# Kernel optimization log

Measured on AMD Instinct MI355X. Metric: run time of the kernel, lower is better.

The kernel has to match this reference:

```python
import jax, jax.numpy as jnp
import numpy as np

V = 256        # vocab (bytes)
DM = 1024      # d_model
NL = 8         # num layers
N = 16         # d_state
K = 4          # d_conv
E = 2 * DM     # d_inner (expand=2)
R = DM // 16   # dt_rank = 64
EPS = 1e-5
B, T = 1, 1024


def setup_inputs() -> dict:
    key = jax.random.key(0)
    ks = jax.random.split(key, 10)
    s = lambda i, shape, scale=0.02: jax.random.normal(ks[i], shape, jnp.float32) * scale
    A_init = jnp.log(jnp.tile(jnp.arange(1, N + 1, dtype=jnp.float32), (NL, E, 1)))
    return {
        "input_ids": jax.random.randint(ks[0], (B, T), 0, V),
        "embed": s(1, (V, DM)),
        "Wxz": s(2, (NL, DM, 2 * E)),            # in_proj (no bias)
        "conv_w": s(3, (NL, E, K), 0.1),          # depthwise causal conv
        "conv_b": jnp.zeros((NL, E), jnp.float32),
        "Wx": s(4, (NL, E, R + 2 * N)),           # x_proj -> dt, B, C
        "Wdt": s(5, (NL, R, E), 0.1),             # dt_proj
        "dt_bias": jnp.full((NL, E), -4.6, jnp.float32),  # softplus(-4.6) ~ 0.01
        "A_log": A_init,                          # A = -exp(A_log), S4D-real init
        "D": jnp.ones((NL, E), jnp.float32),      # skip connection
        "Wout": s(6, (NL, E, DM)),                # out_proj (no bias)
        "norm_w": jnp.ones((NL, DM), jnp.float32),
        "final_norm_w": jnp.ones((DM,), jnp.float32),
        "lm_head_w": s(7, (DM, V)),               # lm_head (no bias)
    }


def rmsnorm(x, w):
    return x * jax.lax.rsqrt(jnp.mean(x * x, axis=-1, keepdims=True) + EPS) * w


def selective_scan(x, dt, A, Bm, Cm, Dp):
    # x, dt: [B,T,E]; A: [E,N]; Bm, Cm: [B,T,N]; Dp: [E]
    dA = jnp.exp(dt[..., None] * A)                              # [B,T,E,N]
    dBx = dt[..., None] * Bm[:, :, None, :] * x[..., None]       # [B,T,E,N]

    def step(h, inp):
        dA_t, dBx_t, C_t = inp                                   # [B,E,N],[B,E,N],[B,N]
        h = dA_t * h + dBx_t
        y = jnp.einsum('ben,bn->be', h, C_t)
        return h, y

    h0 = jnp.zeros((x.shape[0], E, N), x.dtype)
    _, ys = jax.lax.scan(step, h0, (dA.transpose(1, 0, 2, 3),
                                    dBx.transpose(1, 0, 2, 3),
                                    Cm.transpose(1, 0, 2)))
    return ys.transpose(1, 0, 2) + Dp * x                        # [B,T,E]


def mamba_layer(h, p):
    Wxz, cw, cb, Wx, Wdt, dtb, A_log, Dp, Wout, nw = p
    res = h
    u = rmsnorm(h, nw)
    xz = u @ Wxz                                                 # [B,T,2E]
    x, z = jnp.split(xz, 2, axis=-1)
    # causal depthwise conv over time
    xc = jax.lax.conv_general_dilated(x.transpose(0, 2, 1), cw[:, None, :],
                                      (1,), [(K - 1, 0)], feature_group_count=E)
    x = jax.nn.silu(xc.transpose(0, 2, 1) + cb)                  # [B,T,E]
    xdbl = x @ Wx                                                # [B,T,R+2N]
    dt = jax.nn.softplus(xdbl[..., :R] @ Wdt + dtb)              # [B,T,E]
    Bm = xdbl[..., R:R + N]
    Cm = xdbl[..., R + N:]
    A = -jnp.exp(A_log)                                          # [E,N]
    y = selective_scan(x, dt, A, Bm, Cm, Dp)
    y = y * jax.nn.silu(z)
    return res + y @ Wout, None


def reference(input_ids, embed, Wxz, conv_w, conv_b, Wx, Wdt, dt_bias, A_log, D,
              Wout, norm_w, final_norm_w, lm_head_w):
    h = embed[input_ids]                                         # [B,T,DM]
    h, _ = jax.lax.scan(mamba_layer, h,
                        (Wxz, conv_w, conv_b, Wx, Wdt, dt_bias, A_log, D, Wout, norm_w))
    h = rmsnorm(h, final_norm_w)
    return h @ lm_head_w                                         # logits [B,T,V]
```

## Files before the change

kernel.cpp:

```cpp
#include <hip/hip_runtime.h>
#include <hip/hip_bf16.h>

#define DM_   1024
#define NLAY  8
#define NST   16
#define KCONV 4
#define EE    2048
#define E2    4096
#define RNK   64
#define SEQ   1024
#define NXD   96
#define VOC   256
#define EPS_  1e-5f
#define NCH   32
#define CLEN  32

typedef __attribute__((ext_vector_type(8))) short bf16x8;
typedef __attribute__((ext_vector_type(4))) float f32x4;
typedef __hip_bfloat16 bf16;

__device__ __forceinline__ float sigmoidf_(float x){ return 1.f/(1.f+__expf(-x)); }
__device__ __forceinline__ float siluf_(float x){ return x*sigmoidf_(x); }
__device__ __forceinline__ float softplusf_(float x){ return (x>15.f)?x:log1pf(__expf(x)); }

__device__ __forceinline__ void gld_lds16(const short* g, short* lds_uniform){
  __builtin_amdgcn_global_load_lds(
      (const __attribute__((address_space(1))) unsigned int*)(const void*)g,
      (__attribute__((address_space(3))) unsigned int*)(void*)lds_uniform,
      16, 0, 0);
}

__global__ void k_transpose_bf16(const float* __restrict__ in, bf16* __restrict__ out,
                                 int rows, int cols, long in_stride, long out_stride){
  __shared__ float tile[32][33];
  const float* inp = in + (size_t)blockIdx.z * in_stride;
  bf16* outp = out + (size_t)blockIdx.z * out_stride;
  int c0 = blockIdx.x*32, r0 = blockIdx.y*32;
  int tx = threadIdx.x, ty = threadIdx.y;
#pragma unroll
  for (int j = 0; j < 4; j++)
    tile[ty + j*8][tx] = inp[(size_t)(r0 + ty + j*8)*cols + c0 + tx];
  __syncthreads();
#pragma unroll
  for (int j = 0; j < 4; j++)
    outp[(size_t)(c0 + ty + j*8)*rows + r0 + tx] = __float2bfloat16(tile[tx][ty + j*8]);
}

__global__ void k_rmsnorm_fuse(const int* __restrict__ ids, const float* __restrict__ emb,
                               float* __restrict__ h, const float* __restrict__ s0,
                               const float* __restrict__ s1, const float* __restrict__ w,
                               bf16* __restrict__ u){
  int t = blockIdx.x;
  float* hp = h + (size_t)t*DM_;
  float v[4];
  float ss = 0.f;
#pragma unroll
  for (int j = 0; j < 4; j++){
    int i = threadIdx.x + j*256;
    float x;
    if (ids){ x = emb[(size_t)ids[t]*DM_ + i]; hp[i] = x; }
    else if (s0){ x = hp[i] + s0[(size_t)t*DM_ + i] + s1[(size_t)t*DM_ + i]; hp[i] = x; }
    else { x = hp[i]; }
    v[j] = x; ss += x*x;
  }
#pragma unroll
  for (int o = 32; o > 0; o >>= 1) ss += __shfl_down(ss, o, 64);
  __shared__ float red[4];
  if ((threadIdx.x & 63) == 0) red[threadIdx.x >> 6] = ss;
  __syncthreads();
  float tot = red[0]+red[1]+red[2]+red[3];
  float sc = rsqrtf(tot*(1.f/DM_) + EPS_);
  bf16* up = u + (size_t)t*DM_;
#pragma unroll
  for (int j = 0; j < 4; j++){
    int i = threadIdx.x + j*256;
    up[i] = __float2bfloat16(v[j]*sc*w[i]);
  }
}

template<int BM, int BN, int NWM, int NWN, int MODE>
__global__ __launch_bounds__(256) void k_gemm(
    const short* __restrict__ A, const short* __restrict__ Bt, float* __restrict__ C,
    int M, int N, int K, int Ksplit, const float* __restrict__ bias)
{
  constexpr int BK = 64;
  constexpr int WM = BM/NWM, WN = BN/NWN;
  constexpr int MT = WM/16, NT = WN/16;
  constexpr int ABY = BM*BK*2, BBY = BN*BK*2;
  constexpr int AISS = ABY/4096, BISS = BBY/4096;
  __shared__ __align__(16) short As[2][BM*BK];
  __shared__ __align__(16) short Bs[2][BN*BK];
  int tid = threadIdx.x, lane = tid & 63, wave = tid >> 6;
  int wr = wave / NWN, wc = wave % NWN;
  int m0 = blockIdx.x * BM, n0 = blockIdx.y * BN;
  int lrow = lane & 15, lq = lane >> 4;
  int wbase = (tid & ~63) * 16;

  int kbeg = blockIdx.z * Ksplit;
  int nk = Ksplit / BK;

  f32x4 acc[MT][NT];
#pragma unroll
  for (int i = 0; i < MT; i++)
#pragma unroll
    for (int j = 0; j < NT; j++) acc[i][j] = (f32x4){0.f,0.f,0.f,0.f};

  auto stage = [&](int k0, int buf){
#pragma unroll
    for (int i = 0; i < AISS; i++){
      int off = i*4096 + tid*16;
      int row = off >> 7;
      int kc  = ((off >> 4) & 7) ^ (row & 7);
      gld_lds16(A + (size_t)(m0+row)*K + k0 + kc*8,
                As[buf] + ((i*4096 + wbase) >> 1));
    }
#pragma unroll
    for (int i = 0; i < BISS; i++){
      int off = i*4096 + tid*16;
      int row = off >> 7;
      int kc  = ((off >> 4) & 7) ^ (row & 7);
      gld_lds16(Bt + (size_t)(n0+row)*K + k0 + kc*8,
                Bs[buf] + ((i*4096 + wbase) >> 1));
    }
  };

  stage(kbeg, 0);
  __syncthreads();
  for (int it = 0; it < nk; it++){
    int cur = it & 1;
    if (it + 1 < nk) stage(kbeg + (it+1)*BK, cur ^ 1);
#pragma unroll
    for (int s = 0; s < 2; s++){
      bf16x8 af[MT], bfr[NT];
#pragma unroll
      for (int mt = 0; mt < MT; mt++){
        int row = wr*WM + mt*16 + lrow;
        int cc = (s*4 + lq) ^ (row & 7);
        af[mt] = *(const bf16x8*)(As[cur] + row*BK + cc*8);
      }
#pragma unroll
      for (int nt = 0; nt < NT; nt++){
        int row = wc*WN + nt*16 + lrow;
        int cc = (s*4 + lq) ^ (row & 7);
        bfr[nt] = *(const bf16x8*)(Bs[cur] + row*BK + cc*8);
      }
#pragma unroll
      for (int mt = 0; mt < MT; mt++)
#pragma unroll
        for (int nt = 0; nt < NT; nt++)
          acc[mt][nt] = __builtin_amdgcn_mfma_f32_16x16x32_bf16(af[mt], bfr[nt], acc[mt][nt], 0,0,0);
    }
    __syncthreads();
  }

  size_t slab = (MODE == 4) ? (size_t)blockIdx.z * M * N : 0;
#pragma unroll
  for (int mt = 0; mt < MT; mt++){
    int row = m0 + wr*WM + mt*16 + lq*4;
#pragma unroll
    for (int nt = 0; nt < NT; nt++){
      int col = n0 + wc*WN + nt*16 + lrow;
#pragma unroll
      for (int r = 0; r < 4; r++){
        float v = acc[mt][nt][r];
        size_t idx = slab + (size_t)(row + r)*N + col;
        if (MODE == 1) C[idx] = softplusf_(v + bias[col]);
        else C[idx] = v;
      }
    }
  }
}

__global__ void k_conv_silu(const float* __restrict__ xz, const float* __restrict__ cw,
                            const float* __restrict__ cb, float* __restrict__ xact,
                            bf16* __restrict__ xbf){
  int t = blockIdx.y;
  int e = blockIdx.x*256 + threadIdx.x;
  float4 w4 = *(const float4*)(cw + (size_t)e*4);
  float acc = cb[e];
  if (t >= 3){
    acc += xz[(size_t)(t-3)*E2 + e]*w4.x + xz[(size_t)(t-2)*E2 + e]*w4.y
         + xz[(size_t)(t-1)*E2 + e]*w4.z + xz[(size_t)t*E2 + e]*w4.w;
  } else {
    const float* wp = (const float*)&w4;
#pragma unroll
    for (int k = 0; k < 4; k++){ int tt = t-3+k; if (tt >= 0) acc += xz[(size_t)tt*E2 + e]*wp[k]; }
  }
  float xv = siluf_(acc);
  xact[(size_t)t*EE + e] = xv;
  xbf[(size_t)t*EE + e] = __float2bfloat16(xv);
}

__global__ void k_reduce_xdbl(const float* __restrict__ s, float* __restrict__ out,
                              bf16* __restrict__ out64){
  int i = blockIdx.x*256 + threadIdx.x;
  float v = 0.f;
#pragma unroll
  for (int c = 0; c < 8; c++) v += s[(size_t)c*SEQ*NXD + i];
  out[i] = v;
  int t = i / NXD, cc = i - t*NXD;
  if (cc < RNK) out64[(size_t)t*RNK + cc] = __float2bfloat16(v);
}

__global__ void k_reduce_lm(const float* __restrict__ s, float* __restrict__ out){
  int i = blockIdx.x*256 + threadIdx.x;
  float v = 0.f;
#pragma unroll
  for (int c = 0; c < 4; c++) v += s[(size_t)c*SEQ*VOC + i];
  out[i] = v;
}

__global__ void k_scanA(const float* __restrict__ dt, const float* __restrict__ x,
                        const float* __restrict__ xdbl, const float* __restrict__ Alog,
                        float* __restrict__ S, float* __restrict__ dtsum){
  int e = blockIdx.x*256 + threadIdx.x;
  int c = blockIdx.y;
  int t0 = c*CLEN;
  float Ae[NST];
#pragma unroll
  for (int n = 0; n < NST; n++) Ae[n] = -__expf(Alog[(size_t)e*NST + n]);
  __shared__ float Bsm[CLEN][NST];
  for (int i = threadIdx.x; i < CLEN*NST; i += 256)
    Bsm[i>>4][i&15] = xdbl[(size_t)(t0 + (i>>4))*NXD + RNK + (i&15)];
  __syncthreads();
  float h[NST];
#pragma unroll
  for (int n = 0; n < NST; n++) h[n] = 0.f;
  float ds = 0.f;
  for (int tt = 0; tt < CLEN; tt++){
    float dtv = dt[(size_t)(t0+tt)*EE + e];
    float xv  = x[(size_t)(t0+tt)*EE + e];
    ds += dtv;
    float sx = dtv * xv;
#pragma unroll
    for (int n = 0; n < NST; n++)
      h[n] = __expf(dtv*Ae[n])*h[n] + sx*Bsm[tt][n];
  }
  float* Sp = S + ((size_t)c*EE + e)*NST;
#pragma unroll
  for (int n = 0; n < NST; n++) Sp[n] = h[n];
  dtsum[(size_t)c*EE + e] = ds;
}

__global__ void k_scanB(const float* __restrict__ S, const float* __restrict__ dtsum,
                        const float* __restrict__ Alog, float* __restrict__ hinit){
  int idx = blockIdx.x*256 + threadIdx.x;
  float An = -__expf(Alog[idx]);
  int e = idx >> 4;
  float h = 0.f;
  for (int c = 0; c < NCH; c++){
    hinit[(size_t)c*EE*NST + idx] = h;
    h = __expf(dtsum[(size_t)c*EE + e]*An)*h + S[(size_t)c*EE*NST + idx];
  }
}

__global__ void k_scanC(const float* __restrict__ dt, const float* __restrict__ x,
                        const float* __restrict__ xdbl, const float* __restrict__ Alog,
                        const float* __restrict__ Dp, const float* __restrict__ hinit,
                        const float* __restrict__ xz, bf16* __restrict__ ybf){
  int e = blockIdx.x*256 + threadIdx.x;
  int c = blockIdx.y;
  int t0 = c*CLEN;
  float Ae[NST];
#pragma unroll
  for (int n = 0; n < NST; n++) Ae[n] = -__expf(Alog[(size_t)e*NST + n]);
  __shared__ float Bsm[CLEN][NST], Csm[CLEN][NST];
  for (int i = threadIdx.x; i < CLEN*NST; i += 256){
    int tt = i>>4, n = i&15;
    Bsm[tt][n] = xdbl[(size_t)(t0+tt)*NXD + RNK + n];
    Csm[tt][n] = xdbl[(size_t)(t0+tt)*NXD + RNK + NST + n];
  }
  __syncthreads();
  float h[NST];
  const float* hp = hinit + ((size_t)c*EE + e)*NST;
#pragma unroll
  for (int n = 0; n < NST; n++) h[n] = hp[n];
  float Dv = Dp[e];
  for (int tt = 0; tt < CLEN; tt++){
    float dtv = dt[(size_t)(t0+tt)*EE + e];
    float xv  = x[(size_t)(t0+tt)*EE + e];
    float sx = dtv*xv;
    float y = Dv*xv;
#pragma unroll
    for (int n = 0; n < NST; n++){
      h[n] = __expf(dtv*Ae[n])*h[n] + sx*Bsm[tt][n];
      y += h[n]*Csm[tt][n];
    }
    float zv = xz[(size_t)(t0+tt)*E2 + EE + e];
    y *= zv*sigmoidf_(zv);
    ybf[(size_t)(t0+tt)*EE + e] = __float2bfloat16(y);
  }
}

extern "C" void kernel_launch(void* const* d_in, const int* in_sizes, int n_in,
                              void* d_out, int out_size, void* d_ws, size_t ws_size,
                              hipStream_t stream)
{
  const int*   ids  = (const int*)d_in[0];
  const float* emb  = (const float*)d_in[1];
  const float* Wxz  = (const float*)d_in[2];
  const float* cw   = (const float*)d_in[3];
  const float* cb   = (const float*)d_in[4];
  const float* Wx   = (const float*)d_in[5];
  const float* Wdt  = (const float*)d_in[6];
  const float* dtb  = (const float*)d_in[7];
  const float* Alog = (const float*)d_in[8];
  const float* Dp   = (const float*)d_in[9];
  const float* Wout = (const float*)d_in[10];
  const float* nw   = (const float*)d_in[11];
  const float* fnw  = (const float*)d_in[12];
  const float* lmw  = (const float*)d_in[13];

  char* p = (char*)d_ws;
  auto alloc = [&](size_t bytes){ void* r = (void*)p; p += (bytes + 255) & ~(size_t)255; return r; };
  bf16* wxz_bf  = (bf16*)alloc((size_t)NLAY*E2*DM_*2);
  bf16* wout_bf = (bf16*)alloc((size_t)NLAY*DM_*EE*2);
  bf16* wx_bf   = (bf16*)alloc((size_t)NLAY*NXD*EE*2);
  bf16* wdt_bf  = (bf16*)alloc((size_t)NLAY*EE*RNK*2);
  bf16* lm_bf   = (bf16*)alloc((size_t)VOC*DM_*2);
  float* h      = (float*)alloc((size_t)SEQ*DM_*4);
  float* hslab  = (float*)alloc((size_t)2*SEQ*DM_*4);
  bf16* u_bf    = (bf16*)alloc((size_t)SEQ*DM_*2);
  float* xzb    = (float*)alloc((size_t)SEQ*E2*4);
  float* xact   = (float*)alloc((size_t)SEQ*EE*4);
  bf16* x_bf    = (bf16*)alloc((size_t)SEQ*EE*2);
  float* xdbl_s = (float*)alloc((size_t)8*SEQ*NXD*4);
  float* xdbl   = (float*)alloc((size_t)SEQ*NXD*4);
  bf16* xd64    = (bf16*)alloc((size_t)SEQ*RNK*2);
  float* dtbuf  = (float*)alloc((size_t)SEQ*EE*4);
  float* Sbuf   = (float*)alloc((size_t)NCH*EE*NST*4);
  float* dtsum  = (float*)alloc((size_t)NCH*EE*4);
  float* hinit  = (float*)alloc((size_t)NCH*EE*NST*4);
  bf16* y_bf    = (bf16*)alloc((size_t)SEQ*EE*2);
  float* lmslab = (float*)alloc((size_t)4*SEQ*VOC*4);

  k_transpose_bf16<<<dim3(E2/32, DM_/32, NLAY), dim3(32,8), 0, stream>>>(Wxz, wxz_bf, DM_, E2, (long)DM_*E2, (long)E2*DM_);
  k_transpose_bf16<<<dim3(DM_/32, EE/32, NLAY), dim3(32,8), 0, stream>>>(Wout, wout_bf, EE, DM_, (long)EE*DM_, (long)DM_*EE);
  k_transpose_bf16<<<dim3(NXD/32, EE/32, NLAY), dim3(32,8), 0, stream>>>(Wx, wx_bf, EE, NXD, (long)EE*NXD, (long)NXD*EE);
  k_transpose_bf16<<<dim3(EE/32, RNK/32, NLAY), dim3(32,8), 0, stream>>>(Wdt, wdt_bf, RNK, EE, (long)RNK*EE, (long)EE*RNK);
  k_transpose_bf16<<<dim3(VOC/32, DM_/32, 1), dim3(32,8), 0, stream>>>(lmw, lm_bf, DM_, VOC, 0, 0);

  for (int l = 0; l < NLAY; l++){
    k_rmsnorm_fuse<<<SEQ, 256, 0, stream>>>(
        l == 0 ? ids : nullptr, emb, h,
        l == 0 ? nullptr : hslab, hslab + (size_t)SEQ*DM_,
        nw + (size_t)l*DM_, u_bf);
    k_gemm<128,64,2,2,0><<<dim3(SEQ/128, E2/64, 1), 256, 0, stream>>>(
        (const short*)u_bf, (const short*)(wxz_bf + (size_t)l*E2*DM_), xzb,
        SEQ, E2, DM_, DM_, nullptr);
    k_conv_silu<<<dim3(EE/256, SEQ), 256, 0, stream>>>(
        xzb, cw + (size_t)l*EE*KCONV, cb + (size_t)l*EE, xact, x_bf);
    k_gemm<32,96,2,2,4><<<dim3(SEQ/32, 1, 8), 256, 0, stream>>>(
        (const short*)x_bf, (const short*)(wx_bf + (size_t)l*NXD*EE), xdbl_s,
        SEQ, NXD, EE, EE/8, nullptr);
    k_reduce_xdbl<<<SEQ*NXD/256, 256, 0, stream>>>(xdbl_s, xdbl, xd64);
    k_gemm<64,64,2,2,1><<<dim3(SEQ/64, EE/64, 1), 256, 0, stream>>>(
        (const short*)xd64, (const short*)(wdt_bf + (size_t)l*EE*RNK), dtbuf,
        SEQ, EE, RNK, RNK, dtb + (size_t)l*EE);
    k_scanA<<<dim3(EE/256, NCH), 256, 0, stream>>>(
        dtbuf, xact, xdbl, Alog + (size_t)l*EE*NST, Sbuf, dtsum);
    k_scanB<<<dim3(EE*NST/256), 256, 0, stream>>>(Sbuf, dtsum, Alog + (size_t)l*EE*NST, hinit);
    k_scanC<<<dim3(EE/256, NCH), 256, 0, stream>>>(
        dtbuf, xact, xdbl, Alog + (size_t)l*EE*NST, Dp + (size_t)l*EE, hinit, xzb, y_bf);
    k_gemm<64,64,2,2,4><<<dim3(SEQ/64, DM_/64, 2), 256, 0, stream>>>(
        (const short*)y_bf, (const short*)(wout_bf + (size_t)l*DM_*EE), hslab,
        SEQ, DM_, EE, EE/2, nullptr);
  }
  k_rmsnorm_fuse<<<SEQ, 256, 0, stream>>>(
      nullptr, emb, h, hslab, hslab + (size_t)SEQ*DM_, fnw, u_bf);
  k_gemm<64,64,2,2,4><<<dim3(SEQ/64, VOC/64, 4), 256, 0, stream>>>(
      (const short*)u_bf, (const short*)lm_bf, lmslab,
      SEQ, VOC, DM_, DM_/4, nullptr);
  k_reduce_lm<<<SEQ*VOC/256, 256, 0, stream>>>(lmslab, (float*)d_out);
}
```

Measured before the change: 1.164 ms.

## Fuse dt projection into scan pass, atomic split-K reductions, merge weight transposes

Folds the five weight-transpose launches into one grid-strided prep kernel. Replaces the split-K slab-plus-reduce pattern for x_proj and lm_head with atomicAdd into buffers zeroed by earlier kernels. Fuses the dt_proj GEMM and softplus with the chunk-local scan in a single kernel. Removes the scanB pass by having each scanC chunk recompute its starting state from all prior chunk summaries. Launch count and intermediate traffic drop, but scanC takes on a serial prefix loop whose length grows with chunk index, and atomics make summation order nondeterministic.

```diff
diff --git a/kernel.cpp b/kernel.cpp
--- a/kernel.cpp
+++ b/kernel.cpp
@@ -4,7 +4,6 @@
 #define DM_   1024
 #define NLAY  8
 #define NST   16
-#define KCONV 4
 #define EE    2048
 #define E2    4096
 #define RNK   64
@@ -14,14 +13,17 @@
 #define EPS_  1e-5f
 #define NCH   32
 #define CLEN  32
+#define NTHR  256
 
 typedef __attribute__((ext_vector_type(8))) short bf16x8;
 typedef __attribute__((ext_vector_type(4))) float f32x4;
 typedef __hip_bfloat16 bf16;
 
 __device__ __forceinline__ float sigmoidf_(float x){ return 1.f/(1.f+__expf(-x)); }
-__device__ __forceinline__ float siluf_(float x){ return x*sigmoidf_(x); }
 __device__ __forceinline__ float softplusf_(float x){ return (x>15.f)?x:log1pf(__expf(x)); }
+__device__ __forceinline__ short f2bf_s(float x){
+  union { bf16 b; short s; } cv; cv.b = __float2bfloat16(x); return cv.s;
+}
 
 __device__ __forceinline__ void gld_lds16(const short* g, short* lds_uniform){
   __builtin_amdgcn_global_load_lds(
@@ -30,26 +32,46 @@
       16, 0, 0);
 }
 
-__global__ void k_transpose_bf16(const float* __restrict__ in, bf16* __restrict__ out,
-                                 int rows, int cols, long in_stride, long out_stride){
-  __shared__ float tile[32][33];
-  const float* inp = in + (size_t)blockIdx.z * in_stride;
-  bf16* outp = out + (size_t)blockIdx.z * out_stride;
-  int c0 = blockIdx.x*32, r0 = blockIdx.y*32;
-  int tx = threadIdx.x, ty = threadIdx.y;
-#pragma unroll
-  for (int j = 0; j < 4; j++)
-    tile[ty + j*8][tx] = inp[(size_t)(r0 + ty + j*8)*cols + c0 + tx];
-  __syncthreads();
-#pragma unroll
-  for (int j = 0; j < 4; j++)
-    outp[(size_t)(c0 + ty + j*8)*rows + r0 + tx] = __float2bfloat16(tile[tx][ty + j*8]);
+__device__ void t_job(const float* in, bf16* out, int R, int C, int L, char* smem, int gdim){
+  float (*tile)[33] = (float(*)[33])smem;
+  int tC = C >> 5, tR = R >> 5;
+  int per = tC * tR, total = per * L;
+  int tx = threadIdx.x & 31, ty = threadIdx.x >> 5;
+  for (int it = blockIdx.x; it < total; it += gdim){
+    int l = it / per, rem = it - l*per;
+    int tc = rem % tC, tr = rem / tC;
+    const float* inp = in + (size_t)l*R*C;
+    bf16* outp = out + (size_t)l*R*C;
+    int c0 = tc*32, r0 = tr*32;
+    __syncthreads();
+#pragma unroll
+    for (int j = 0; j < 4; j++)
+      tile[ty + j*8][tx] = inp[(size_t)(r0+ty+j*8)*C + c0+tx];
+    __syncthreads();
+#pragma unroll
+    for (int j = 0; j < 4; j++)
+      outp[(size_t)(c0+ty+j*8)*R + r0+tx] = __float2bfloat16(tile[tx][ty+j*8]);
+  }
+}
+
+__global__ __launch_bounds__(256) void k_prep(
+    const float* __restrict__ Wxz, const float* __restrict__ Wout,
+    const float* __restrict__ Wx, const float* __restrict__ Wdt,
+    const float* __restrict__ lmw,
+    bf16* wxz_bf, bf16* wout_bf, bf16* wx_bf, bf16* wdt_bf, bf16* lm_bf){
+  __shared__ __align__(16) char smem[4352];
+  int gdim = gridDim.x;
+  t_job(Wxz,  wxz_bf,  DM_, E2,  NLAY, smem, gdim);
+  t_job(Wout, wout_bf, EE,  DM_, NLAY, smem, gdim);
+  t_job(Wx,   wx_bf,   EE,  NXD, NLAY, smem, gdim);
+  t_job(Wdt,  wdt_bf,  RNK, EE,  NLAY, smem, gdim);
+  t_job(lmw,  lm_bf,   DM_, VOC, 1,    smem, gdim);
 }
 
 __global__ void k_rmsnorm_fuse(const int* __restrict__ ids, const float* __restrict__ emb,
                                float* __restrict__ h, const float* __restrict__ s0,
                                const float* __restrict__ s1, const float* __restrict__ w,
-                               bf16* __restrict__ u){
+                               bf16* __restrict__ u, float* __restrict__ zout){
   int t = blockIdx.x;
   float* hp = h + (size_t)t*DM_;
   float v[4];
@@ -59,8 +81,7 @@
     int i = threadIdx.x + j*256;
     float x;
     if (ids){ x = emb[(size_t)ids[t]*DM_ + i]; hp[i] = x; }
-    else if (s0){ x = hp[i] + s0[(size_t)t*DM_ + i] + s1[(size_t)t*DM_ + i]; hp[i] = x; }
-    else { x = hp[i]; }
+    else { x = hp[i] + s0[(size_t)t*DM_ + i] + s1[(size_t)t*DM_ + i]; hp[i] = x; }
     v[j] = x; ss += x*x;
   }
 #pragma unroll
@@ -76,12 +97,13 @@
     int i = threadIdx.x + j*256;
     up[i] = __float2bfloat16(v[j]*sc*w[i]);
   }
+  if (zout) zout[(size_t)t*VOC + threadIdx.x] = 0.f;
 }
 
 template<int BM, int BN, int NWM, int NWN, int MODE>
 __global__ __launch_bounds__(256) void k_gemm(
     const short* __restrict__ A, const short* __restrict__ Bt, float* __restrict__ C,
-    int M, int N, int K, int Ksplit, const float* __restrict__ bias)
+    int M, int N, int K, int Ksplit)
 {
   constexpr int BK = 64;
   constexpr int WM = BM/NWM, WN = BN/NWN;
@@ -111,16 +133,14 @@
       int off = i*4096 + tid*16;
       int row = off >> 7;
       int kc  = ((off >> 4) & 7) ^ (row & 7);
-      gld_lds16(A + (size_t)(m0+row)*K + k0 + kc*8,
-                As[buf] + ((i*4096 + wbase) >> 1));
+      gld_lds16(A + (size_t)(m0+row)*K + k0 + kc*8, As[buf] + ((i*4096 + wbase) >> 1));
     }
 #pragma unroll
     for (int i = 0; i < BISS; i++){
       int off = i*4096 + tid*16;
       int row = off >> 7;
       int kc  = ((off >> 4) & 7) ^ (row & 7);
-      gld_lds16(Bt + (size_t)(n0+row)*K + k0 + kc*8,
-                Bs[buf] + ((i*4096 + wbase) >> 1));
+      gld_lds16(Bt + (size_t)(n0+row)*K + k0 + kc*8, Bs[buf] + ((i*4096 + wbase) >> 1));
     }
   };
 
@@ -164,7 +184,7 @@
       for (int r = 0; r < 4; r++){
         float v = acc[mt][nt][r];
         size_t idx = slab + (size_t)(row + r)*N + col;
-        if (MODE == 1) C[idx] = softplusf_(v + bias[col]);
+        if (MODE == 5) atomicAdd(&C[idx], v);
         else C[idx] = v;
       }
     }
@@ -173,7 +193,7 @@
 
 __global__ void k_conv_silu(const float* __restrict__ xz, const float* __restrict__ cw,
                             const float* __restrict__ cb, float* __restrict__ xact,
-                            bf16* __restrict__ xbf){
+                            bf16* __restrict__ xbf, float* __restrict__ xdbl){
   int t = blockIdx.y;
   int e = blockIdx.x*256 + threadIdx.x;
   float4 w4 = *(const float4*)(cw + (size_t)e*4);
@@ -186,78 +206,136 @@
 #pragma unroll
     for (int k = 0; k < 4; k++){ int tt = t-3+k; if (tt >= 0) acc += xz[(size_t)tt*E2 + e]*wp[k]; }
   }
-  float xv = siluf_(acc);
-  xact[(size_t)t*EE + e] = xv;
-  xbf[(size_t)t*EE + e] = __float2bfloat16(xv);
-}
-
-__global__ void k_reduce_xdbl(const float* __restrict__ s, float* __restrict__ out,
-                              bf16* __restrict__ out64){
-  int i = blockIdx.x*256 + threadIdx.x;
-  float v = 0.f;
-#pragma unroll
-  for (int c = 0; c < 8; c++) v += s[(size_t)c*SEQ*NXD + i];
-  out[i] = v;
-  int t = i / NXD, cc = i - t*NXD;
-  if (cc < RNK) out64[(size_t)t*RNK + cc] = __float2bfloat16(v);
-}
-
-__global__ void k_reduce_lm(const float* __restrict__ s, float* __restrict__ out){
-  int i = blockIdx.x*256 + threadIdx.x;
-  float v = 0.f;
-#pragma unroll
-  for (int c = 0; c < 4; c++) v += s[(size_t)c*SEQ*VOC + i];
-  out[i] = v;
-}
-
-__global__ void k_scanA(const float* __restrict__ dt, const float* __restrict__ x,
-                        const float* __restrict__ xdbl, const float* __restrict__ Alog,
-                        float* __restrict__ S, float* __restrict__ dtsum){
-  int e = blockIdx.x*256 + threadIdx.x;
-  int c = blockIdx.y;
-  int t0 = c*CLEN;
-  float Ae[NST];
-#pragma unroll
-  for (int n = 0; n < NST; n++) Ae[n] = -__expf(Alog[(size_t)e*NST + n]);
-  __shared__ float Bsm[CLEN][NST];
-  for (int i = threadIdx.x; i < CLEN*NST; i += 256)
-    Bsm[i>>4][i&15] = xdbl[(size_t)(t0 + (i>>4))*NXD + RNK + (i&15)];
-  __syncthreads();
-  float h[NST];
-#pragma unroll
-  for (int n = 0; n < NST; n++) h[n] = 0.f;
-  float ds = 0.f;
-  for (int tt = 0; tt < CLEN; tt++){
-    float dtv = dt[(size_t)(t0+tt)*EE + e];
-    float xv  = x[(size_t)(t0+tt)*EE + e];
-    ds += dtv;
-    float sx = dtv * xv;
-#pragma unroll
-    for (int n = 0; n < NST; n++)
-      h[n] = __expf(dtv*Ae[n])*h[n] + sx*Bsm[tt][n];
-  }
-  float* Sp = S + ((size_t)c*EE + e)*NST;
-#pragma unroll
-  for (int n = 0; n < NST; n++) Sp[n] = h[n];
-  dtsum[(size_t)c*EE + e] = ds;
-}
-
-__global__ void k_scanB(const float* __restrict__ S, const float* __restrict__ dtsum,
-                        const float* __restrict__ Alog, float* __restrict__ hinit){
-  int idx = blockIdx.x*256 + threadIdx.x;
-  float An = -__expf(Alog[idx]);
-  int e = idx >> 4;
-  float h = 0.f;
-  for (int c = 0; c < NCH; c++){
-    hinit[(size_t)c*EE*NST + idx] = h;
-    h = __expf(dtsum[(size_t)c*EE + e]*An)*h + S[(size_t)c*EE*NST + idx];
+  float xv = acc * sigmoidf_(acc);
+  size_t id = (size_t)t*EE + e;
+  xact[id] = xv;
+  xbf[id] = __float2bfloat16(xv);
+  if (id < SEQ*NXD) xdbl[id] = 0.f;
+}
+
+__global__ __launch_bounds__(256) void k_dt_scanA(
+    const float* __restrict__ xdbl, const short* __restrict__ WdtT,
+    const float* __restrict__ dtb, const float* __restrict__ Alog,
+    const float* __restrict__ xact, float* __restrict__ dtbuf,
+    float* __restrict__ S, float* __restrict__ dtsum)
+{
+  __shared__ __align__(16) char smem[22528];
+  short* As = (short*)smem;
+  short* Bs = (short*)(smem + 8192);
+  float (*dts)[65]  = (float(*)[65])smem;
+  float (*Bcol)[17] = (float(*)[17])(smem + 16640);
+  int tid = threadIdx.x;
+  int lane = tid & 63, wave = tid >> 6;
+  int wr = wave >> 1, wc = wave & 1, lrow = lane & 15, lq = lane >> 4;
+  int m0 = blockIdx.x*64, n0 = blockIdx.y*64;
+
+  {
+    int row = tid >> 2;
+    int kq  = (tid & 3) << 4;
+    const float* src = xdbl + (size_t)(m0+row)*NXD + kq;
+    short tmp[16] __attribute__((aligned(16)));
+#pragma unroll
+    for (int j = 0; j < 16; j++) tmp[j] = f2bf_s(src[j]);
+    int c0 = ((kq>>3) + 0) ^ (row & 7);
+    int c1 = ((kq>>3) + 1) ^ (row & 7);
+    *(bf16x8*)(As + row*64 + c0*8) = *(const bf16x8*)(tmp);
+    *(bf16x8*)(As + row*64 + c1*8) = *(const bf16x8*)(tmp + 8);
+  }
+  {
+    int wbase = (tid & ~63) * 16;
+#pragma unroll
+    for (int i = 0; i < 2; i++){
+      int off = i*4096 + tid*16;
+      int row = off >> 7;
+      int kc  = ((off >> 4) & 7) ^ (row & 7);
+      gld_lds16(WdtT + (size_t)(n0+row)*RNK + kc*8, Bs + ((i*4096 + wbase) >> 1));
+    }
+  }
+  __syncthreads();
+  f32x4 acc[2][2];
+#pragma unroll
+  for (int i = 0; i < 2; i++)
+#pragma unroll
+    for (int j = 0; j < 2; j++) acc[i][j] = (f32x4){0.f,0.f,0.f,0.f};
+#pragma unroll
+  for (int s = 0; s < 2; s++){
+    bf16x8 af[2], bfr[2];
+#pragma unroll
+    for (int mt = 0; mt < 2; mt++){
+      int row = wr*32 + mt*16 + lrow;
+      int cc = (s*4 + lq) ^ (row & 7);
+      af[mt] = *(const bf16x8*)(As + row*64 + cc*8);
+    }
+#pragma unroll
+    for (int nt = 0; nt < 2; nt++){
+      int row = wc*32 + nt*16 + lrow;
+      int cc = (s*4 + lq) ^ (row & 7);
+      bfr[nt] = *(const bf16x8*)(Bs + row*64 + cc*8);
+    }
+#pragma unroll
+    for (int mt = 0; mt < 2; mt++)
+#pragma unroll
+      for (int nt = 0; nt < 2; nt++)
+        acc[mt][nt] = __builtin_amdgcn_mfma_f32_16x16x32_bf16(af[mt], bfr[nt], acc[mt][nt], 0,0,0);
+  }
+  __syncthreads();
+
+#pragma unroll
+  for (int mt = 0; mt < 2; mt++){
+    int rl = wr*32 + mt*16 + lq*4;
+#pragma unroll
+    for (int nt = 0; nt < 2; nt++){
+      int cl = wc*32 + nt*16 + lrow;
+#pragma unroll
+      for (int r = 0; r < 4; r++){
+        float v = softplusf_(acc[mt][nt][r] + dtb[n0 + cl]);
+        dtbuf[(size_t)(m0 + rl + r)*EE + n0 + cl] = v;
+        dts[rl + r][cl] = v;
+      }
+    }
+  }
+  {
+    int row = tid >> 2, n4 = (tid & 3) << 2;
+    float4 b4 = *(const float4*)(xdbl + (size_t)(m0+row)*NXD + RNK + n4);
+    Bcol[row][n4+0] = b4.x; Bcol[row][n4+1] = b4.y;
+    Bcol[row][n4+2] = b4.z; Bcol[row][n4+3] = b4.w;
+  }
+  __syncthreads();
+
+  if (tid < 128){
+    int ch = tid >> 6, el = tid & 63;
+    int e = n0 + el;
+    int c = (m0 >> 5) + ch;
+    int t0 = c*CLEN;
+    const float* Al = Alog + (size_t)e*NST;
+    float Ae[NST];
+#pragma unroll
+    for (int n = 0; n < NST; n++) Ae[n] = -__expf(Al[n]);
+    float h[NST];
+#pragma unroll
+    for (int n = 0; n < NST; n++) h[n] = 0.f;
+    float ds = 0.f;
+    for (int tt = 0; tt < CLEN; tt++){
+      float dtv = dts[ch*CLEN + tt][el];
+      float xv  = xact[(size_t)(t0+tt)*EE + e];
+      ds += dtv;
+      float sx = dtv*xv;
+#pragma unroll
+      for (int n = 0; n < NST; n++)
+        h[n] = __expf(dtv*Ae[n])*h[n] + sx*Bcol[ch*CLEN + tt][n];
+    }
+    float* Sp = S + ((size_t)c*EE + e)*NST;
+#pragma unroll
+    for (int n = 0; n < NST; n++) Sp[n] = h[n];
+    dtsum[(size_t)c*EE + e] = ds;
   }
 }
 
 __global__ void k_scanC(const float* __restrict__ dt, const float* __restrict__ x,
                         const float* __restrict__ xdbl, const float* __restrict__ Alog,
-                        const float* __restrict__ Dp, const float* __restrict__ hinit,
-                        const float* __restrict__ xz, bf16* __restrict__ ybf){
+                        const float* __restrict__ Dp, const float* __restrict__ S,
+                        const float* __restrict__ dtsum, const float* __restrict__ xz,
+                        bf16* __restrict__ ybf){
   int e = blockIdx.x*256 + threadIdx.x;
   int c = blockIdx.y;
   int t0 = c*CLEN;
@@ -272,9 +350,15 @@
   }
   __syncthreads();
   float h[NST];
-  const float* hp = hinit + ((size_t)c*EE + e)*NST;
-#pragma unroll
-  for (int n = 0; n < NST; n++) h[n] = hp[n];
+#pragma unroll
+  for (int n = 0; n < NST; n++) h[n] = 0.f;
+  for (int j = 0; j < c; j++){
+    float dsj = dtsum[(size_t)j*EE + e];
+    const float* Sj = S + ((size_t)j*EE + e)*NST;
+#pragma unroll
+    for (int n = 0; n < NST; n++)
+      h[n] = __expf(dsj*Ae[n])*h[n] + Sj[n];
+  }
   float Dv = Dp[e];
   for (int tt = 0; tt < CLEN; tt++){
     float dtv = dt[(size_t)(t0+tt)*EE + e];
@@ -324,52 +408,41 @@
   float* xzb    = (float*)alloc((size_t)SEQ*E2*4);
   float* xact   = (float*)alloc((size_t)SEQ*EE*4);
   bf16* x_bf    = (bf16*)alloc((size_t)SEQ*EE*2);
-  float* xdbl_s = (float*)alloc((size_t)8*SEQ*NXD*4);
   float* xdbl   = (float*)alloc((size_t)SEQ*NXD*4);
-  bf16* xd64    = (bf16*)alloc((size_t)SEQ*RNK*2);
   float* dtbuf  = (float*)alloc((size_t)SEQ*EE*4);
   float* Sbuf   = (float*)alloc((size_t)NCH*EE*NST*4);
   float* dtsum  = (float*)alloc((size_t)NCH*EE*4);
-  float* hinit  = (float*)alloc((size_t)NCH*EE*NST*4);
   bf16* y_bf    = (bf16*)alloc((size_t)SEQ*EE*2);
-  float* lmslab = (float*)alloc((size_t)4*SEQ*VOC*4);
-
-  k_transpose_bf16<<<dim3(E2/32, DM_/32, NLAY), dim3(32,8), 0, stream>>>(Wxz, wxz_bf, DM_, E2, (long)DM_*E2, (long)E2*DM_);
-  k_transpose_bf16<<<dim3(DM_/32, EE/32, NLAY), dim3(32,8), 0, stream>>>(Wout, wout_bf, EE, DM_, (long)EE*DM_, (long)DM_*EE);
-  k_transpose_bf16<<<dim3(NXD/32, EE/32, NLAY), dim3(32,8), 0, stream>>>(Wx, wx_bf, EE, NXD, (long)EE*NXD, (long)NXD*EE);
-  k_transpose_bf16<<<dim3(EE/32, RNK/32, NLAY), dim3(32,8), 0, stream>>>(Wdt, wdt_bf, RNK, EE, (long)RNK*EE, (long)EE*RNK);
-  k_transpose_bf16<<<dim3(VOC/32, DM_/32, 1), dim3(32,8), 0, stream>>>(lmw, lm_bf, DM_, VOC, 0, 0);
+
+  k_prep<<<512, 256, 0, stream>>>(Wxz, Wout, Wx, Wdt, lmw,
+                                  wxz_bf, wout_bf, wx_bf, wdt_bf, lm_bf);
 
   for (int l = 0; l < NLAY; l++){
     k_rmsnorm_fuse<<<SEQ, 256, 0, stream>>>(
         l == 0 ? ids : nullptr, emb, h,
-        l == 0 ? nullptr : hslab, hslab + (size_t)SEQ*DM_,
-        nw + (size_t)l*DM_, u_bf);
+        hslab, hslab + (size_t)SEQ*DM_,
+        nw + (size_t)l*DM_, u_bf, nullptr);
     k_gemm<128,64,2,2,0><<<dim3(SEQ/128, E2/64, 1), 256, 0, stream>>>(
         (const short*)u_bf, (const short*)(wxz_bf + (size_t)l*E2*DM_), xzb,
-        SEQ, E2, DM_, DM_, nullptr);
+        SEQ, E2, DM_, DM_);
     k_conv_silu<<<dim3(EE/256, SEQ), 256, 0, stream>>>(
-        xzb, cw + (size_t)l*EE*KCONV, cb + (size_t)l*EE, xact, x_bf);
-    k_gemm<32,96,2,2,4><<<dim3(SEQ/32, 1, 8), 256, 0, stream>>>(
-        (const short*)x_bf, (const short*)(wx_bf + (size_t)l*NXD*EE), xdbl_s,
-        SEQ, NXD, EE, EE/8, nullptr);
-    k_reduce_xdbl<<<SEQ*NXD/256, 256, 0, stream>>>(xdbl_s, xdbl, xd64);
-    k_gemm<64,64,2,2,1><<<dim3(SEQ/64, EE/64, 1), 256, 0, stream>>>(
-        (const short*)xd64, (const short*)(wdt_bf + (size_t)l*EE*RNK), dtbuf,
-        SEQ, EE, RNK, RNK, dtb + (size_t)l*EE);
-    k_scanA<<<dim3(EE/256, NCH), 256, 0, stream>>>(
-        dtbuf, xact, xdbl, Alog + (size_t)l*EE*NST, Sbuf, dtsum);
-    k_scanB<<<dim3(EE*NST/256), 256, 0, stream>>>(Sbuf, dtsum, Alog + (size_t)l*EE*NST, hinit);
+        xzb, cw + (size_t)l*EE*4, cb + (size_t)l*EE, xact, x_bf, xdbl);
+    k_gemm<32,96,2,2,5><<<dim3(SEQ/32, 1, 16), 256, 0, stream>>>(
+        (const short*)x_bf, (const short*)(wx_bf + (size_t)l*NXD*EE), xdbl,
+        SEQ, NXD, EE, EE/16);
+    k_dt_scanA<<<dim3(SEQ/64, EE/64), 256, 0, stream>>>(
+        xdbl, (const short*)(wdt_bf + (size_t)l*EE*RNK), dtb + (size_t)l*EE,
+        Alog + (size_t)l*EE*NST, xact, dtbuf, Sbuf, dtsum);
     k_scanC<<<dim3(EE/256, NCH), 256, 0, stream>>>(
-        dtbuf, xact, xdbl, Alog + (size_t)l*EE*NST, Dp + (size_t)l*EE, hinit, xzb, y_bf);
+        dtbuf, xact, xdbl, Alog + (size_t)l*EE*NST, Dp + (size_t)l*EE,
+        Sbuf, dtsum, xzb, y_bf);
     k_gemm<64,64,2,2,4><<<dim3(SEQ/64, DM_/64, 2), 256, 0, stream>>>(
         (const short*)y_bf, (const short*)(wout_bf + (size_t)l*DM_*EE), hslab,
-        SEQ, DM_, EE, EE/2, nullptr);
+        SEQ, DM_, EE, EE/2);
   }
   k_rmsnorm_fuse<<<SEQ, 256, 0, stream>>>(
-      nullptr, emb, h, hslab, hslab + (size_t)SEQ*DM_, fnw, u_bf);
-  k_gemm<64,64,2,2,4><<<dim3(SEQ/64, VOC/64, 4), 256, 0, stream>>>(
-      (const short*)u_bf, (const short*)lm_bf, lmslab,
-      SEQ, VOC, DM_, DM_/4, nullptr);
-  k_reduce_lm<<<SEQ*VOC/256, 256, 0, stream>>>(lmslab, (float*)d_out);
-}
+      nullptr, emb, h, hslab, hslab + (size_t)SEQ*DM_, fnw, u_bf, (float*)d_out);
+  k_gemm<64,64,2,2,5><<<dim3(SEQ/64, VOC/64, 4), 256, 0, stream>>>(
+      (const short*)u_bf, (const short*)lm_bf, (float*)d_out,
+      SEQ, VOC, DM_, DM_/4);
+}
```

Measured after the change: 1.237 ms. 6.2% more time.
